# Performance work log

Hardware: AMD Instinct MI355X
Metric: run time of the kernel (lower is better)

The kernel has to match this reference:

```python
import jax, jax.numpy as jnp
import numpy as np

SEQ, D_A, H, D_K, D_V = 4096, 2048, 16, 128, 128


def setup_inputs() -> dict:
    key = jax.random.key(0)
    ks = jax.random.split(key, 7)
    return {
        "queries": jax.random.normal(ks[0], (SEQ, D_A), dtype=jnp.float32),
        "keys":    jax.random.normal(ks[1], (SEQ, D_A), dtype=jnp.float32),
        "values":  jax.random.normal(ks[2], (SEQ, D_A), dtype=jnp.float32),
        "Eq": jax.random.normal(ks[3], (H, D_A, D_K), dtype=jnp.float32),
        "Ek": jax.random.normal(ks[4], (H, D_A, D_K), dtype=jnp.float32),
        "Ev": jax.random.normal(ks[5], (H, D_A, D_V), dtype=jnp.float32),
        "W_out": jax.random.normal(ks[6], (H * D_V, D_A), dtype=jnp.float32),
    }


def reference(queries, keys, values, Eq, Ek, Ev, W_out):
    # Per-head projections: [seq, d_a] x [h, d_a, d] -> [h, seq, d]
    Q = jnp.einsum("sd,hdk->hsk", queries, Eq)
    K = jnp.einsum("sd,hdk->hsk", keys, Ek)
    V = jnp.einsum("sd,hdv->hsv", values, Ev)
    scale = 1.0 / D_K  # faithful to source: 1/d_k, not 1/sqrt(d_k)
    dots = jnp.einsum("hqk,hsk->hqs", Q, K) * scale  # [h, seq, seq]
    attn = jax.nn.softmax(dots, axis=-1)  # dropout p=0 -> identity
    out = jnp.einsum("hqs,hsv->hqv", attn, V)  # [h, seq, d_v]
    # concat heads along last dim: [seq, h*d_v]
    A = jnp.transpose(out, (1, 0, 2)).reshape(SEQ, H * D_V)
    return A @ W_out  # [seq, d_a]
```

## Files before the change

### kernel.cpp

```cpp
#include <hip/hip_runtime.h>

typedef unsigned short u16;
typedef __attribute__((ext_vector_type(4)))  float  f32x4;
typedef __attribute__((ext_vector_type(16))) float  f32x16;
typedef __attribute__((ext_vector_type(4)))  float  float4v;
typedef __attribute__((ext_vector_type(4)))  unsigned short u16x4;
typedef __attribute__((ext_vector_type(8)))  unsigned short u16x8;
typedef __attribute__((ext_vector_type(8)))  short s16x8;
typedef __attribute__((ext_vector_type(4)))  unsigned int u32x4;

#define SEQ 4096
#define DA  2048
#define NH  16
#define DKV 128

__device__ __forceinline__ u16 f2bf(float f) {
    unsigned u = __builtin_bit_cast(unsigned, f);
    u += 0x7FFFu + ((u >> 16) & 1u);
    return (u16)(u >> 16);
}
__device__ __forceinline__ float bf2f(u16 h) {
    return __builtin_bit_cast(float, (unsigned)h << 16);
}
__device__ __forceinline__ f32x4 mfma16(u16x8 a, u16x8 b, f32x4 c) {
    return __builtin_amdgcn_mfma_f32_16x16x32_bf16(
        __builtin_bit_cast(s16x8, a), __builtin_bit_cast(s16x8, b), c, 0, 0, 0);
}
__device__ __forceinline__ f32x16 mfma32(u16x8 a, u16x8 b, f32x16 c) {
    return __builtin_amdgcn_mfma_f32_32x32x16_bf16(
        __builtin_bit_cast(s16x8, a), __builtin_bit_cast(s16x8, b), c, 0, 0, 0);
}
__device__ __forceinline__ unsigned cvtpk(float lo, float hi) {
    unsigned r;
    asm("v_cvt_pk_bf16_f32 %0, %1, %2" : "=v"(r) : "v"(lo), "v"(hi));
    return r;
}
__device__ __forceinline__ void gld16(const u16* g, u16* l) {
    __builtin_amdgcn_global_load_lds(
        (const __attribute__((address_space(1))) unsigned int*)g,
        (__attribute__((address_space(3))) unsigned int*)l, 16, 0, 0);
}
__device__ __forceinline__ char* ldsp(void* base, int row, int bcol, int rowbytes) {
    int off = row * rowbytes + bcol;
    off ^= (row & 7) << 4;
    return (char*)base + off;
}
__device__ __forceinline__ char* ldsp256(void* base, int row, int bcol) {
    int off = row * 256 + bcol;
    off ^= (row & 15) << 4;
    return (char*)base + off;
}

__global__ void transpose_split_k(const float* __restrict__ in, u16* __restrict__ oh,
                                  u16* __restrict__ ol, int R, int C) {
    __shared__ float tile[32][33];
    int b  = blockIdx.z;
    int r0 = blockIdx.x * 32, c0 = blockIdx.y * 32;
    const float* src = in + (size_t)b * R * C;
    int t = threadIdx.x;
    {
        int cl = t & 31, r = t >> 5;
        for (int i = 0; i < 4; ++i)
            tile[r + 8 * i][cl] = src[(size_t)(r0 + r + 8 * i) * C + (c0 + cl)];
    }
    __syncthreads();
    int rl = t & 31, c = t >> 5;
    size_t obase = (size_t)b * R * C;
    for (int i = 0; i < 4; ++i) {
        int cw = c + 8 * i;
        float x = tile[rl][cw];
        u16 h = f2bf(x);
        size_t o = obase + (size_t)(c0 + cw) * R + (r0 + rl);
        oh[o] = h;
        if (ol) ol[o] = f2bf(x - bf2f(h));
    }
}

template <int MODE>
__global__ void __launch_bounds__(256, 2) proj_k(const float* __restrict__ A,
                                                 const u16* __restrict__ BTh,
                                                 const u16* __restrict__ BTl,
                                                 u16* __restrict__ Oh,
                                                 u16* __restrict__ Ol) {
    __shared__ u16 sAh[128 * 64];
    __shared__ u16 sBh[128 * 64];
    __shared__ u16 sAl[MODE ? 128 * 64 : 8];
    __shared__ u16 sBl[MODE ? 128 * 64 : 8];

    int t = threadIdx.x;
    int h = blockIdx.y;
    int bm0 = blockIdx.x * 128;
    int lane = t & 63, w = t >> 6, wr = w >> 1, wc = w & 1;
    int g = lane >> 4, c = lane & 15;

    f32x4 acc[4][4] = {};

    float4v pA[8];
    u16x8   pBh[4], pBl[4];

    auto prefetch = [&](int k0) {
#pragma unroll
        for (int i = 0; i < 8; ++i) {
            int idx = t + i * 256;
            int row = idx >> 4, c4 = idx & 15;
            pA[i] = *(const float4v*)(A + (size_t)(bm0 + row) * DA + k0 + c4 * 4);
        }
#pragma unroll
        for (int i = 0; i < 4; ++i) {
            int idx = t + i * 256;
            int row = idx >> 3, c8 = idx & 7;
            size_t gb = ((size_t)h * 128 + row) * DA + k0 + c8 * 8;
            pBh[i] = *(const u16x8*)(BTh + gb);
            if (MODE) pBl[i] = *(const u16x8*)(BTl + gb);
        }
    };
    auto write_lds = [&]() {
#pragma unroll
        for (int i = 0; i < 8; ++i) {
            int idx = t + i * 256;
            int row = idx >> 4, c4 = idx & 15;
            u16x4 hv, lv;
#pragma unroll
            for (int j = 0; j < 4; ++j) {
                u16 hh = f2bf(pA[i][j]);
                hv[j] = hh;
                lv[j] = f2bf(pA[i][j] - bf2f(hh));
            }
            *(u16x4*)ldsp(sAh, row, c4 * 8, 128) = hv;
            if (MODE) *(u16x4*)ldsp(sAl, row, c4 * 8, 128) = lv;
        }
#pragma unroll
        for (int i = 0; i < 4; ++i) {
            int idx = t + i * 256;
            int row = idx >> 3, c8 = idx & 7;
            *(u16x8*)ldsp(sBh, row, c8 * 16, 128) = pBh[i];
            if (MODE) *(u16x8*)ldsp(sBl, row, c8 * 16, 128) = pBl[i];
        }
    };

    prefetch(0);
    for (int k0 = 0; k0 < DA; k0 += 64) {
        __syncthreads();
        write_lds();
        __syncthreads();
        int nxt = (k0 + 64 < DA) ? k0 + 64 : 0;
        prefetch(nxt);

        for (int kc = 0; kc < 2; ++kc) {
            int kb = (kc * 32 + g * 8) * 2;
            u16x8 ah[4], al[4], bh[4], bl[4];
            for (int m = 0; m < 4; ++m) {
                int row = wr * 64 + m * 16 + c;
                ah[m] = *(u16x8*)ldsp(sAh, row, kb, 128);
                if (MODE) al[m] = *(u16x8*)ldsp(sAl, row, kb, 128);
            }
            for (int n = 0; n < 4; ++n) {
                int row = wc * 64 + n * 16 + c;
                bh[n] = *(u16x8*)ldsp(sBh, row, kb, 128);
                if (MODE) bl[n] = *(u16x8*)ldsp(sBl, row, kb, 128);
            }
            for (int m = 0; m < 4; ++m)
                for (int n = 0; n < 4; ++n) {
                    acc[m][n] = mfma16(ah[m], bh[n], acc[m][n]);
                    if (MODE) {
                        acc[m][n] = mfma16(ah[m], bl[n], acc[m][n]);
                        acc[m][n] = mfma16(al[m], bh[n], acc[m][n]);
                    }
                }
        }
    }

    const float scale = (MODE == 2) ? (1.0f / 128.0f) : 1.0f;
    for (int m = 0; m < 4; ++m)
        for (int n = 0; n < 4; ++n) {
            int col  = wc * 64 + n * 16 + c;
            int row0 = bm0 + wr * 64 + m * 16 + g * 4;
            if (MODE == 0) {
                u16x4 pv;
                for (int j = 0; j < 4; ++j) pv[j] = f2bf(acc[m][n][j]);
                *(u16x4*)(Oh + ((size_t)h * DKV + col) * SEQ + row0) = pv;
            } else {
                for (int j = 0; j < 4; ++j) {
                    float v = acc[m][n][j] * scale;
                    u16 hh = f2bf(v);
                    size_t o = ((size_t)h * SEQ + row0 + j) * DKV + col;
                    Oh[o] = hh;
                    Ol[o] = f2bf(v - bf2f(hh));
                }
            }
        }
}

__global__ void __launch_bounds__(512, 1) attn_k(const u16* __restrict__ QH,
                                                 const u16* __restrict__ QL,
                                                 const u16* __restrict__ KH,
                                                 const u16* __restrict__ KL,
                                                 const u16* __restrict__ VT,
                                                 u16* __restrict__ Abuf) {
    __shared__ u16 sKh[2][64 * 128];
    __shared__ u16 sKl[2][64 * 128];
    __shared__ u16 sV [2][64 * 128];

    int t = threadIdx.x, lane = t & 63, w = t >> 6;
    int bid = blockIdx.x;
    int h  = (bid & 7) + 8 * ((bid >> 3) & 1);
    int q0 = (bid >> 4) * 256;
    int c = lane & 31, hi = lane >> 5;
    int qrow = q0 + w * 32 + c;

    u16x8 qh[8], ql[8];
    {
        size_t base = ((size_t)h * SEQ + qrow) * DKV + hi * 8;
#pragma unroll
        for (int dc = 0; dc < 8; ++dc) {
            qh[dc] = *(const u16x8*)(QH + base + dc * 16);
            ql[dc] = *(const u16x8*)(QL + base + dc * 16);
        }
    }

    f32x16 o[4] = {};
    float mrun = -3e38f, lrun = 0.f;

    const size_t kroot = (size_t)h * SEQ * DKV;
    const size_t vroot = (size_t)h * DKV * SEQ;

    auto stage = [&](int kv, int b) {
        const u16* khp = KH + kroot + (size_t)kv * DKV;
        const u16* klp = KL + kroot + (size_t)kv * DKV;
        const u16* vtp = VT + vroot + kv;
#pragma unroll
        for (int j = 0; j < 2; ++j) {
            int ci = w * 2 + j;
            int rK = ci * 4 + (lane >> 4);
            int cK = (lane & 15) ^ (rK & 15);
            gld16(khp + rK * DKV + cK * 8, &sKh[b][ci * 512]);
            gld16(klp + rK * DKV + cK * 8, &sKl[b][ci * 512]);
            int vd = ((cK >> 3) << 6) + rK;
            gld16(vtp + (size_t)vd * SEQ + (cK & 7) * 8, &sV[b][ci * 512]);
        }
    };

    stage(0, 0);
    const int NT = SEQ / 64;
    for (int it = 0; it < NT; ++it) {
        int b = it & 1;
        __syncthreads();
        if (it + 1 < NT) stage((it + 1) * 64, b ^ 1);

        f32x16 s[2] = {};
        __builtin_amdgcn_s_setprio(1);
#pragma unroll
        for (int kt = 0; kt < 2; ++kt) {
#pragma unroll
            for (int dc = 0; dc < 8; ++dc) {
                u16x8 kh = *(u16x8*)ldsp256(sKh[b], kt * 32 + c, dc * 32 + hi * 16);
                u16x8 kl = *(u16x8*)ldsp256(sKl[b], kt * 32 + c, dc * 32 + hi * 16);
                s[kt] = mfma32(kh, qh[dc], s[kt]);
                s[kt] = mfma32(kl, qh[dc], s[kt]);
                s[kt] = mfma32(kh, ql[dc], s[kt]);
            }
        }
        __builtin_amdgcn_s_setprio(0);

        float vmax = s[0][0];
#pragma unroll
        for (int r = 1; r < 16; ++r) vmax = fmaxf(vmax, s[0][r]);
#pragma unroll
        for (int r = 0; r < 16; ++r) vmax = fmaxf(vmax, s[1][r]);
        vmax = fmaxf(vmax, __shfl_xor(vmax, 32));
        if (!__all(vmax <= mrun + 8.0f)) {
            float mnew = fmaxf(mrun, vmax);
            float corr = __expf(mrun - mnew);
            mrun = mnew;
            lrun *= corr;
#pragma unroll
            for (int vt = 0; vt < 4; ++vt)
#pragma unroll
                for (int r = 0; r < 16; ++r) o[vt][r] *= corr;
        }
        float rs = 0.f;
#pragma unroll
        for (int kt = 0; kt < 2; ++kt)
#pragma unroll
            for (int r = 0; r < 16; ++r) {
                float p = __expf(s[kt][r] - mrun);
                s[kt][r] = p;
                rs += p;
            }
        rs += __shfl_xor(rs, 32);
        lrun += rs;

#pragma unroll
        for (int kt = 0; kt < 2; ++kt) {
            unsigned wv[8], xw[8];
#pragma unroll
            for (int i = 0; i < 8; ++i) wv[i] = cvtpk(s[kt][2 * i], s[kt][2 * i + 1]);
#pragma unroll
            for (int i = 0; i < 8; ++i) xw[i] = (unsigned)__shfl_xor((int)wv[i], 32);
            __builtin_amdgcn_s_setprio(1);
#pragma unroll
            for (int kc = 0; kc < 2; ++kc) {
                u32x4 pw;
                pw[0] = hi ? xw[4 * kc + 2] : wv[4 * kc + 0];
                pw[1] = hi ? xw[4 * kc + 3] : wv[4 * kc + 1];
                pw[2] = hi ? wv[4 * kc + 2] : xw[4 * kc + 0];
                pw[3] = hi ? wv[4 * kc + 3] : xw[4 * kc + 1];
                u16x8 pf = __builtin_bit_cast(u16x8, pw);
#pragma unroll
                for (int vt = 0; vt < 4; ++vt) {
                    int v = vt * 32 + c;
                    u16x8 vf = *(u16x8*)ldsp256(sV[b], v & 63,
                                                ((v >> 6) << 7) + kt * 64 + kc * 32 + hi * 16);
                    o[vt] = mfma32(vf, pf, o[vt]);
                }
            }
            __builtin_amdgcn_s_setprio(0);
        }
    }

    float inv = 1.0f / lrun;
#pragma unroll
    for (int vt = 0; vt < 4; ++vt)
#pragma unroll
        for (int rg = 0; rg < 4; ++rg) {
            u16x4 pv;
#pragma unroll
            for (int j = 0; j < 4; ++j) pv[j] = f2bf(o[vt][rg * 4 + j] * inv);
            *(u16x4*)(Abuf + (size_t)qrow * (NH * DKV) + h * DKV + vt * 32 + rg * 8 + hi * 4) = pv;
        }
}

__global__ void __launch_bounds__(256, 2) gemm_out_k(const u16* __restrict__ Abuf,
                                                     const u16* __restrict__ WT,
                                                     float* __restrict__ out) {
    __shared__ u16 sA[128 * 64];
    __shared__ u16 sB[128 * 64];
    int t = threadIdx.x, lane = t & 63, w = t >> 6, wr = w >> 1, wc = w & 1;
    int g = lane >> 4, c = lane & 15;
    int bm0 = blockIdx.x * 128, bn0 = blockIdx.y * 128;
    f32x4 acc[4][4] = {};

    u16x8 pA[4], pB[4];
    auto prefetch = [&](int k0) {
#pragma unroll
        for (int i = 0; i < 4; ++i) {
            int idx = t + i * 256, row = idx >> 3, c8 = idx & 7;
            pA[i] = *(const u16x8*)(Abuf + (size_t)(bm0 + row) * DA + k0 + c8 * 8);
            pB[i] = *(const u16x8*)(WT + (size_t)(bn0 + row) * DA + k0 + c8 * 8);
        }
    };
    auto write_lds = [&]() {
#pragma unroll
        for (int i = 0; i < 4; ++i) {
            int idx = t + i * 256, row = idx >> 3, c8 = idx & 7;
            *(u16x8*)ldsp(sA, row, c8 * 16, 128) = pA[i];
            *(u16x8*)ldsp(sB, row, c8 * 16, 128) = pB[i];
        }
    };

    prefetch(0);
    for (int k0 = 0; k0 < DA; k0 += 64) {
        __syncthreads();
        write_lds();
        __syncthreads();
        int nxt = (k0 + 64 < DA) ? k0 + 64 : 0;
        prefetch(nxt);

        for (int kc = 0; kc < 2; ++kc) {
            int kb = (kc * 32 + g * 8) * 2;
            u16x8 af[4], bfq[4];
            for (int m = 0; m < 4; ++m) af[m]  = *(u16x8*)ldsp(sA, wr * 64 + m * 16 + c, kb, 128);
            for (int n = 0; n < 4; ++n) bfq[n] = *(u16x8*)ldsp(sB, wc * 64 + n * 16 + c, kb, 128);
            for (int m = 0; m < 4; ++m)
                for (int n = 0; n < 4; ++n)
                    acc[m][n] = mfma16(af[m], bfq[n], acc[m][n]);
        }
    }
    for (int m = 0; m < 4; ++m)
        for (int n = 0; n < 4; ++n) {
            int row0 = bm0 + wr * 64 + m * 16 + g * 4;
            int col  = bn0 + wc * 64 + n * 16 + c;
            for (int j = 0; j < 4; ++j)
                out[(size_t)(row0 + j) * DA + col] = acc[m][n][j];
        }
}

extern "C" void kernel_launch(void* const* d_in, const int* in_sizes, int n_in,
                              void* d_out, int out_size, void* d_ws, size_t ws_size,
                              hipStream_t stream) {
    const float* queries = (const float*)d_in[0];
    const float* keys    = (const float*)d_in[1];
    const float* values  = (const float*)d_in[2];
    const float* Eq      = (const float*)d_in[3];
    const float* Ek      = (const float*)d_in[4];
    const float* Ev      = (const float*)d_in[5];
    const float* Wout    = (const float*)d_in[6];
    float* out = (float*)d_out;

    const size_t PROJ = (size_t)NH * SEQ * DKV;
    const size_t TSZ  = (size_t)DA * DA;
    u16* p  = (u16*)d_ws;
    u16* QH = p; p += PROJ;
    u16* QL = p; p += PROJ;
    u16* KH = p; p += PROJ;
    u16* KL = p; p += PROJ;
    u16* VT = p; p += PROJ;
    u16* AB = p; p += (size_t)SEQ * NH * DKV;
    u16* TH = p; p += TSZ;
    u16* TL = p; p += TSZ;

    dim3 tgE(DA / 32, DKV / 32, NH);
    dim3 tgW(DA / 32, DA / 32, 1);
    dim3 pg(SEQ / 128, NH);

    transpose_split_k<<<tgE, 256, 0, stream>>>(Eq, TH, TL, DA, DKV);
    proj_k<2><<<pg, 256, 0, stream>>>(queries, TH, TL, QH, QL);
    transpose_split_k<<<tgE, 256, 0, stream>>>(Ek, TH, TL, DA, DKV);
    proj_k<1><<<pg, 256, 0, stream>>>(keys, TH, TL, KH, KL);
    transpose_split_k<<<tgE, 256, 0, stream>>>(Ev, TH, nullptr, DA, DKV);
    proj_k<0><<<pg, 256, 0, stream>>>(values, TH, nullptr, VT, nullptr);
    transpose_split_k<<<tgW, 256, 0, stream>>>(Wout, TH, nullptr, DA, DA);
    attn_k<<<dim3(SEQ / 256 * NH), 512, 0, stream>>>(QH, QL, KH, KL, VT, AB);
    gemm_out_k<<<dim3(SEQ / 128, DA / 128), 256, 0, stream>>>(AB, TH, out);
}
```

Before: 590.6 us.

## Pre-split activations to bf16 and load GEMM tiles via direct global-to-LDS

Adds a standalone kernel that converts fp32 query/key/value activations into bf16 hi/lo planes once, with the query scale folded in. The projection and output GEMMs then stage tiles with gld16 global-to-LDS copies using an XOR-swizzled column layout, replacing the register prefetch plus LDS write path. The aim is to stop redoing the hi/lo split in every one of the 16 head blocks and to cut VGPR and LDS-store traffic. In exchange it adds three extra full passes over the activations and drops the register double-buffering, so global loads no longer overlap with compute inside a block.

```diff
diff --git a/kernel.cpp b/kernel.cpp
--- a/kernel.cpp
+++ b/kernel.cpp
@@ -76,12 +76,31 @@
     }
 }
 
+__global__ void split_cvt_k(const float* __restrict__ in, u16* __restrict__ oh,
+                            u16* __restrict__ ol, float scale, int n) {
+    int stride = gridDim.x * 256 * 4;
+    for (int i = (blockIdx.x * 256 + threadIdx.x) * 4; i < n; i += stride) {
+        float4v v = *(const float4v*)(in + i);
+        u16x4 hv, lv;
+#pragma unroll
+        for (int j = 0; j < 4; ++j) {
+            float x = v[j] * scale;
+            u16 hh = f2bf(x);
+            hv[j] = hh;
+            lv[j] = f2bf(x - bf2f(hh));
+        }
+        *(u16x4*)(oh + i) = hv;
+        if (ol) *(u16x4*)(ol + i) = lv;
+    }
+}
+
 template <int MODE>
-__global__ void __launch_bounds__(256, 2) proj_k(const float* __restrict__ A,
-                                                 const u16* __restrict__ BTh,
-                                                 const u16* __restrict__ BTl,
-                                                 u16* __restrict__ Oh,
-                                                 u16* __restrict__ Ol) {
+__global__ void __launch_bounds__(256, 2) proj2_k(const u16* __restrict__ ASh,
+                                                  const u16* __restrict__ ASl,
+                                                  const u16* __restrict__ BTh,
+                                                  const u16* __restrict__ BTl,
+                                                  u16* __restrict__ Oh,
+                                                  u16* __restrict__ Ol) {
     __shared__ u16 sAh[128 * 64];
     __shared__ u16 sBh[128 * 64];
     __shared__ u16 sAl[MODE ? 128 * 64 : 8];
@@ -93,58 +112,27 @@
     int lane = t & 63, w = t >> 6, wr = w >> 1, wc = w & 1;
     int g = lane >> 4, c = lane & 15;
 
+    int rin = lane >> 3;
+    int cg  = (lane & 7) ^ rin;
+
     f32x4 acc[4][4] = {};
 
-    float4v pA[8];
-    u16x8   pBh[4], pBl[4];
-
-    auto prefetch = [&](int k0) {
-#pragma unroll
-        for (int i = 0; i < 8; ++i) {
-            int idx = t + i * 256;
-            int row = idx >> 4, c4 = idx & 15;
-            pA[i] = *(const float4v*)(A + (size_t)(bm0 + row) * DA + k0 + c4 * 4);
-        }
-#pragma unroll
-        for (int i = 0; i < 4; ++i) {
-            int idx = t + i * 256;
-            int row = idx >> 3, c8 = idx & 7;
-            size_t gb = ((size_t)h * 128 + row) * DA + k0 + c8 * 8;
-            pBh[i] = *(const u16x8*)(BTh + gb);
-            if (MODE) pBl[i] = *(const u16x8*)(BTl + gb);
-        }
-    };
-    auto write_lds = [&]() {
-#pragma unroll
-        for (int i = 0; i < 8; ++i) {
-            int idx = t + i * 256;
-            int row = idx >> 4, c4 = idx & 15;
-            u16x4 hv, lv;
-#pragma unroll
-            for (int j = 0; j < 4; ++j) {
-                u16 hh = f2bf(pA[i][j]);
-                hv[j] = hh;
-                lv[j] = f2bf(pA[i][j] - bf2f(hh));
-            }
-            *(u16x4*)ldsp(sAh, row, c4 * 8, 128) = hv;
-            if (MODE) *(u16x4*)ldsp(sAl, row, c4 * 8, 128) = lv;
-        }
-#pragma unroll
-        for (int i = 0; i < 4; ++i) {
-            int idx = t + i * 256;
-            int row = idx >> 3, c8 = idx & 7;
-            *(u16x8*)ldsp(sBh, row, c8 * 16, 128) = pBh[i];
-            if (MODE) *(u16x8*)ldsp(sBl, row, c8 * 16, 128) = pBl[i];
-        }
-    };
-
-    prefetch(0);
     for (int k0 = 0; k0 < DA; k0 += 64) {
         __syncthreads();
-        write_lds();
+#pragma unroll
+        for (int j = 0; j < 4; ++j) {
+            int chunk = w * 4 + j;
+            int r = chunk * 8 + rin;
+            size_t ga = (size_t)(bm0 + r) * DA + k0 + cg * 8;
+            size_t gb = ((size_t)h * 128 + r) * DA + k0 + cg * 8;
+            gld16(ASh + ga, &sAh[chunk * 512]);
+            gld16(BTh + gb, &sBh[chunk * 512]);
+            if (MODE) {
+                gld16(ASl + ga, &sAl[chunk * 512]);
+                gld16(BTl + gb, &sBl[chunk * 512]);
+            }
+        }
         __syncthreads();
-        int nxt = (k0 + 64 < DA) ? k0 + 64 : 0;
-        prefetch(nxt);
 
         for (int kc = 0; kc < 2; ++kc) {
             int kb = (kc * 32 + g * 8) * 2;
@@ -170,7 +158,6 @@
         }
     }
 
-    const float scale = (MODE == 2) ? (1.0f / 128.0f) : 1.0f;
     for (int m = 0; m < 4; ++m)
         for (int n = 0; n < 4; ++n) {
             int col  = wc * 64 + n * 16 + c;
@@ -181,7 +168,7 @@
                 *(u16x4*)(Oh + ((size_t)h * DKV + col) * SEQ + row0) = pv;
             } else {
                 for (int j = 0; j < 4; ++j) {
-                    float v = acc[m][n][j] * scale;
+                    float v = acc[m][n][j];
                     u16 hh = f2bf(v);
                     size_t o = ((size_t)h * SEQ + row0 + j) * DKV + col;
                     Oh[o] = hh;
@@ -338,33 +325,20 @@
     int t = threadIdx.x, lane = t & 63, w = t >> 6, wr = w >> 1, wc = w & 1;
     int g = lane >> 4, c = lane & 15;
     int bm0 = blockIdx.x * 128, bn0 = blockIdx.y * 128;
+    int rin = lane >> 3;
+    int cg  = (lane & 7) ^ rin;
     f32x4 acc[4][4] = {};
 
-    u16x8 pA[4], pB[4];
-    auto prefetch = [&](int k0) {
-#pragma unroll
-        for (int i = 0; i < 4; ++i) {
-            int idx = t + i * 256, row = idx >> 3, c8 = idx & 7;
-            pA[i] = *(const u16x8*)(Abuf + (size_t)(bm0 + row) * DA + k0 + c8 * 8);
-            pB[i] = *(const u16x8*)(WT + (size_t)(bn0 + row) * DA + k0 + c8 * 8);
-        }
-    };
-    auto write_lds = [&]() {
-#pragma unroll
-        for (int i = 0; i < 4; ++i) {
-            int idx = t + i * 256, row = idx >> 3, c8 = idx & 7;
-            *(u16x8*)ldsp(sA, row, c8 * 16, 128) = pA[i];
-            *(u16x8*)ldsp(sB, row, c8 * 16, 128) = pB[i];
-        }
-    };
-
-    prefetch(0);
     for (int k0 = 0; k0 < DA; k0 += 64) {
         __syncthreads();
-        write_lds();
+#pragma unroll
+        for (int j = 0; j < 4; ++j) {
+            int chunk = w * 4 + j;
+            int r = chunk * 8 + rin;
+            gld16(Abuf + (size_t)(bm0 + r) * DA + k0 + cg * 8, &sA[chunk * 512]);
+            gld16(WT   + (size_t)(bn0 + r) * DA + k0 + cg * 8, &sB[chunk * 512]);
+        }
         __syncthreads();
-        int nxt = (k0 + 64 < DA) ? k0 + 64 : 0;
-        prefetch(nxt);
 
         for (int kc = 0; kc < 2; ++kc) {
             int kb = (kc * 32 + g * 8) * 2;
@@ -399,6 +373,7 @@
 
     const size_t PROJ = (size_t)NH * SEQ * DKV;
     const size_t TSZ  = (size_t)DA * DA;
+    const size_t ASZ  = (size_t)SEQ * DA;
     u16* p  = (u16*)d_ws;
     u16* QH = p; p += PROJ;
     u16* QL = p; p += PROJ;
@@ -408,17 +383,23 @@
     u16* AB = p; p += (size_t)SEQ * NH * DKV;
     u16* TH = p; p += TSZ;
     u16* TL = p; p += TSZ;
+    u16* Sh = p; p += ASZ;
+    u16* Sl = p; p += ASZ;
 
     dim3 tgE(DA / 32, DKV / 32, NH);
     dim3 tgW(DA / 32, DA / 32, 1);
     dim3 pg(SEQ / 128, NH);
+    const int NELEM = SEQ * DA;
 
     transpose_split_k<<<tgE, 256, 0, stream>>>(Eq, TH, TL, DA, DKV);
-    proj_k<2><<<pg, 256, 0, stream>>>(queries, TH, TL, QH, QL);
+    split_cvt_k<<<2048, 256, 0, stream>>>(queries, Sh, Sl, 1.0f / 128.0f, NELEM);
+    proj2_k<2><<<pg, 256, 0, stream>>>(Sh, Sl, TH, TL, QH, QL);
     transpose_split_k<<<tgE, 256, 0, stream>>>(Ek, TH, TL, DA, DKV);
-    proj_k<1><<<pg, 256, 0, stream>>>(keys, TH, TL, KH, KL);
+    split_cvt_k<<<2048, 256, 0, stream>>>(keys, Sh, Sl, 1.0f, NELEM);
+    proj2_k<1><<<pg, 256, 0, stream>>>(Sh, Sl, TH, TL, KH, KL);
     transpose_split_k<<<tgE, 256, 0, stream>>>(Ev, TH, nullptr, DA, DKV);
-    proj_k<0><<<pg, 256, 0, stream>>>(values, TH, nullptr, VT, nullptr);
+    split_cvt_k<<<2048, 256, 0, stream>>>(values, Sh, nullptr, 1.0f, NELEM);
+    proj2_k<0><<<pg, 256, 0, stream>>>(Sh, nullptr, TH, nullptr, VT, nullptr);
     transpose_split_k<<<tgW, 256, 0, stream>>>(Wout, TH, nullptr, DA, DA);
     attn_k<<<dim3(SEQ / 256 * NH), 512, 0, stream>>>(QH, QL, KH, KL, VT, AB);
     gemm_out_k<<<dim3(SEQ / 128, DA / 128), 256, 0, stream>>>(AB, TH, out);
```

New measurement: 576.2 us, median of 6. 1.03x faster.
